# Kernel tuning notes

Measured on AMD Instinct MI355X. Metric: run time of the kernel, lower is better.

Reference implementation:

```python
import jax, jax.numpy as jnp
import numpy as np

B, C, H, W = 4, 1024, 14, 14
L = 80          # num labels / graph nodes
WD = 300        # word embedding dim
INTER = 1024    # semantic intermediary dim
OUT = 2048      # output_dim
TIME_STEP = 3


def setup_inputs() -> dict:
    key = jax.random.key(0)
    ks = jax.random.split(key, 24)
    s = 0.02  # weight scale to keep gates/tanh in sane range
    return {
        "img_feature_map": jax.random.normal(ks[0], (B, C, H, W), jnp.float32),
        "word_embedding": jax.random.normal(ks[1], (L, WD), jnp.float32),
        "adjacency": jax.random.uniform(ks[2], (L, L), jnp.float32) / L,
        "fc1_w": jax.random.normal(ks[3], (INTER, C), jnp.float32) * s,
        "fc2_w": jax.random.normal(ks[4], (INTER, WD), jnp.float32) * s,
        "fc3_w": jax.random.normal(ks[5], (INTER, INTER), jnp.float32) * s,
        "fc3_b": jnp.zeros((INTER,), jnp.float32),
        "fca_w": jax.random.normal(ks[6], (1, INTER), jnp.float32) * s,
        "fca_b": jnp.zeros((1,), jnp.float32),
        "w3": jax.random.normal(ks[7], (C, 2 * C), jnp.float32) * s,
        "b3": jnp.zeros((C,), jnp.float32),
        "u3": jax.random.normal(ks[8], (C, C), jnp.float32) * s,
        "u3b": jnp.zeros((C,), jnp.float32),
        "w4": jax.random.normal(ks[9], (C, 2 * C), jnp.float32) * s,
        "b4": jnp.zeros((C,), jnp.float32),
        "w5": jax.random.normal(ks[10], (C, 2 * C), jnp.float32) * s,
        "b5": jnp.zeros((C,), jnp.float32),
        "u5": jax.random.normal(ks[11], (C, C), jnp.float32) * s,
        "u5b": jnp.zeros((C,), jnp.float32),
        "fco_w": jax.random.normal(ks[12], (OUT, 2 * C), jnp.float32) * s,
        "fco_b": jnp.zeros((OUT,), jnp.float32),
    }


def _semantic(fmap, word_emb, fc1_w, fc2_w, fc3_w, fc3_b, fca_w, fca_b):
    # Faithful to torch: view(-1, C) on a contiguous (B,C,H,W) tensor is a raw
    # row-major reinterpret (NOT a BHWC transpose). jnp.reshape matches.
    b, c, h, w = fmap.shape
    x = fmap.reshape(-1, c)                                   # (B*H*W, C)
    f_wh = x @ fc1_w.T                                        # (N, INTER)
    f_wd = word_emb @ fc2_w.T                                 # (L, INTER)
    lb = jnp.tanh(f_wh[:, None, :] * f_wd[None, :, :])        # (N, L, INTER)
    lb = lb @ fc3_w.T + fc3_b                                 # (N, L, INTER)
    coeff = lb @ fca_w.T + fca_b                              # (N, L, 1)
    coeff = coeff.reshape(b, L, h * w)                        # torch .view semantics
    coeff = jax.nn.softmax(coeff, axis=2)
    coeff = coeff.reshape(b, h, w, L)
    fmap_bhwc = fmap.reshape(b, h, w, c)                      # raw reinterpret, as torch
    return jnp.einsum('bhwl,bhwc->blc', coeff, fmap_bhwc)     # (B, L, C)


def _ggnn(nodes, adj, w3, b3, u3, u3b, w4, b4, w5, b5, u5, u5b):
    for _ in range(TIME_STEP):
        a = jnp.einsum('nm,bmd->bnd', adj, nodes)             # in == out matrix
        av = jnp.concatenate([a, a], axis=-1)                 # (B, L, 2C)
        u3x = nodes @ u3.T + u3b
        z = jax.nn.sigmoid(av @ w3.T + b3 + u3x)
        r = jax.nn.sigmoid(av @ w4.T + b4 + u3x)              # torch bug: reuses fc_eq3_u
        hcand = jnp.tanh(av @ w5.T + b5 + (r * nodes) @ u5.T + u5b)
        nodes = (1.0 - z) * nodes + z * hcand
    return nodes


def reference(img_feature_map, word_embedding, adjacency,
              fc1_w, fc2_w, fc3_w, fc3_b, fca_w, fca_b,
              w3, b3, u3, u3b, w4, b4, w5, b5, u5, u5b,
              fco_w, fco_b):
    g = _semantic(img_feature_map, word_embedding,
                  fc1_w, fc2_w, fc3_w, fc3_b, fca_w, fca_b)   # (B, L, C)
    nodes = _ggnn(g, adjacency, w3, b3, u3, u3b, w4, b4, w5, b5, u5, u5b)
    feat = jnp.concatenate([nodes, g], axis=-1)               # (B, L, 2C)
    out = jnp.tanh(feat @ fco_w.T + fco_b)                    # (B, L, OUT)
    return out
```

## Files before the change

kernel.cpp:

```cpp
#include <hip/hip_runtime.h>
#include <hip/hip_bf16.h>

#define LL 80
#define NPIX 784
#define PBATCH 15680

#define DI __device__ __forceinline__

typedef short s8v __attribute__((ext_vector_type(8)));
typedef short short4v __attribute__((ext_vector_type(4)));
typedef float f32x4 __attribute__((ext_vector_type(4)));

DI float b2f(__hip_bfloat16 x) { return __bfloat162float(x); }
DI float s2f(short h) { return __uint_as_float(((unsigned int)(unsigned short)h) << 16); }

DI short f2b(float x) {
    unsigned int b = __float_as_uint(x);
    b += 0x7fffu + ((b >> 16) & 1u);
    return (short)(b >> 16);
}

template <int F> DI float LD(const void* p, int i) {
    if (F) return ((const float*)p)[i];
    return b2f(((const __hip_bfloat16*)p)[i]);
}

DI float fast_tanh(float x) {
    float e = __expf(2.0f * x);
    return 1.0f - 2.0f / (e + 1.0f);
}
DI float fast_sigmoid(float x) { return 1.0f / (1.0f + __expf(-x)); }

__global__ __launch_bounds__(256) void detect_dtype(const void* probe, int n, int* flag) {
    __shared__ int bad;
    if (threadIdx.x == 0) bad = 0;
    __syncthreads();
    int c = 0;
    for (int i = threadIdx.x; i < n; i += 256) {
        float v = b2f(((const __hip_bfloat16*)probe)[i]);
        if (!(fabsf(v) < 1000.0f)) c++;
    }
    if (c) atomicAdd(&bad, c);
    __syncthreads();
    if (threadIdx.x == 0) *flag = (bad > 8) ? 1 : 0;
}

DI void cvt_part(int f, const void* src, short* __restrict__ dst, int blk, int n) {
    int i0 = (blk * 256 + threadIdx.x) * 4;
    if (i0 >= n) return;
    if (f) {
        float4 v = *(const float4*)((const float*)src + i0);
        short4v o = { f2b(v.x), f2b(v.y), f2b(v.z), f2b(v.w) };
        *(short4v*)(dst + i0) = o;
    } else {
        *(short4v*)(dst + i0) = *(const short4v*)((const short*)src + i0);
    }
}

DI void wcat_part(int f, const void* w3, const void* w4, const void* w5, const void* u3,
                  short* __restrict__ wcat, int blk) {
    int i0 = (blk * 256 + threadIdx.x) * 4;
    int nr = i0 >> 10, k = i0 & 1023;
    int j = nr >> 10, r = nr & 1023;
    const void* W = (j == 0) ? w3 : (j == 1) ? w4 : (j == 2) ? w5 : u3;
    float4 v;
    if (j < 3) {
        if (f) {
            float4 x = *(const float4*)((const float*)W + r * 2048 + k);
            float4 y = *(const float4*)((const float*)W + r * 2048 + 1024 + k);
            v.x = x.x + y.x; v.y = x.y + y.y; v.z = x.z + y.z; v.w = x.w + y.w;
        } else {
            const short* Ws = (const short*)W;
            short4v x = *(const short4v*)(Ws + r * 2048 + k);
            short4v y = *(const short4v*)(Ws + r * 2048 + 1024 + k);
            v.x = s2f(x.x) + s2f(y.x); v.y = s2f(x.y) + s2f(y.y);
            v.z = s2f(x.z) + s2f(y.z); v.w = s2f(x.w) + s2f(y.w);
        }
    } else {
        if (f) v = *(const float4*)((const float*)W + r * 1024 + k);
        else {
            short4v x = *(const short4v*)((const short*)W + r * 1024 + k);
            v.x = s2f(x.x); v.y = s2f(x.y); v.z = s2f(x.z); v.w = s2f(x.w);
        }
    }
    short4v o = { f2b(v.x), f2b(v.y), f2b(v.z), f2b(v.w) };
    *(short4v*)(wcat + i0) = o;
}

template <int F>
DI void prep_u_part(const void* fc3_w, const void* fc3_b,
                    const void* fca_w, const void* fca_b,
                    float* u, float* c0, float* red, int blk) {
    if (blk < 4) {
        int k = blk * 256 + threadIdx.x;
        float acc = 0.f;
        for (int j = 0; j < 1024; j++)
            acc += LD<F>(fca_w, j) * LD<F>(fc3_w, j * 1024 + k);
        u[k] = acc;
    } else {
        float acc = 0.f;
        for (int j = threadIdx.x; j < 1024; j += 256)
            acc += LD<F>(fc3_b, j) * LD<F>(fca_w, j);
        red[threadIdx.x] = acc;
        __syncthreads();
        for (int s = 128; s > 0; s >>= 1) {
            if (threadIdx.x < s) red[threadIdx.x] += red[threadIdx.x + s];
            __syncthreads();
        }
        if (threadIdx.x == 0) *c0 = red[0] + LD<F>(fca_b, 0);
    }
}

template <int F>
DI void fc2_part(float* lds, const void* word, const void* fc2_w, float* C, int bx, int by) {
    float* As = lds;
    float* Ws2 = lds + 1088;
    const int tid = threadIdx.x;
    const int tx = tid & 15, ty = tid >> 4;
    const int m0 = by * 64, n0 = bx * 64;
    const int M = 80, K = 300;
    float acc[4][4] = {};

    for (int k0 = 0; k0 < K; k0 += 16) {
#pragma unroll
        for (int i = 0; i < 4; i++) {
            int idx = tid + i * 256;
            int kk = idx & 15, mm = idx >> 4;
            int m = m0 + mm, k = k0 + kk;
            As[kk * 68 + mm] = (m < M && k < K) ? LD<F>(word, m * 300 + k) : 0.f;
        }
#pragma unroll
        for (int i = 0; i < 4; i++) {
            int idx = tid + i * 256;
            int kk = idx & 15, nn = idx >> 4;
            int n = n0 + nn, k = k0 + kk;
            Ws2[kk * 68 + nn] = (k < K) ? LD<F>(fc2_w, n * 300 + k) : 0.f;
        }
        __syncthreads();
#pragma unroll
        for (int kk = 0; kk < 16; kk++) {
            float4 av = *(const float4*)(&As[kk * 68 + ty * 4]);
            float4 wv = *(const float4*)(&Ws2[kk * 68 + tx * 4]);
            float a4[4] = {av.x, av.y, av.z, av.w};
            float w4[4] = {wv.x, wv.y, wv.z, wv.w};
#pragma unroll
            for (int i = 0; i < 4; i++)
#pragma unroll
                for (int j = 0; j < 4; j++)
                    acc[i][j] += a4[i] * w4[j];
        }
        __syncthreads();
    }

    for (int i = 0; i < 4; i++) {
        int m = m0 + ty * 4 + i;
        if (m >= M) continue;
        for (int j = 0; j < 4; j++)
            C[m * 1024 + n0 + tx * 4 + j] = acc[i][j];
    }
}

__global__ __launch_bounds__(256) void mega_prep(
    const int* flag,
    const void* fmap, const void* fc1_w, const void* u5w,
    const void* w3, const void* w4, const void* w5, const void* u3,
    const void* fc3_w, const void* fc3_b, const void* fca_w, const void* fca_b,
    const void* word, const void* fc2_w,
    short* fmap_b, short* fc1w_b, short* u5w_b, short* wcat_b,
    float* u, float* c0, float* f_wd) {
    __shared__ float lds[2176];
    int f = *flag;
    int bid = blockIdx.x;
    if      (bid < 784)  cvt_part(f, fmap,  fmap_b, bid,        802816);
    else if (bid < 1808) cvt_part(f, fc1_w, fc1w_b, bid - 784,  1048576);
    else if (bid < 2832) cvt_part(f, u5w,   u5w_b,  bid - 1808, 1048576);
    else if (bid < 6928) wcat_part(f, w3, w4, w5, u3, wcat_b, bid - 2832);
    else if (bid < 6933) {
        if (f) prep_u_part<1>(fc3_w, fc3_b, fca_w, fca_b, u, c0, lds, bid - 6928);
        else   prep_u_part<0>(fc3_w, fc3_b, fca_w, fca_b, u, c0, lds, bid - 6928);
    } else {
        int r = bid - 6933;
        if (f) fc2_part<1>(lds, word, fc2_w, f_wd, r & 15, r >> 4);
        else   fc2_part<0>(lds, word, fc2_w, f_wd, r & 15, r >> 4);
    }
}

__global__ __launch_bounds__(256) void cvt_k(const int* flag, const void* src,
                                             short* __restrict__ dst, int n) {
    cvt_part(*flag, src, dst, blockIdx.x, n);
}

DI void mcore_b(const short* __restrict__ A, int lda,
                const short* __restrict__ B, int ldb,
                float* __restrict__ C, int ldc,
                int M, int kb, int ke, int m0, int n0) {
    __shared__ short As[4][64][8];
    __shared__ short Ws[4][64][8];
    const int tid = threadIdx.x;
    const int wv = tid >> 6, lane = tid & 63;
    const int mA = tid & 63, qA = tid >> 6;
    f32x4 acc[4] = {};

    for (int k0 = kb; k0 < ke; k0 += 32) {
        s8v va = {0,0,0,0,0,0,0,0};
        int gm = m0 + mA;
        if (gm < M) va = *(const s8v*)(A + gm * lda + k0 + 8 * qA);
        *(s8v*)&As[mA >> 4][(mA & 15) | (qA << 4)][0] = va;
        s8v vb = *(const s8v*)(B + (n0 + mA) * ldb + k0 + 8 * qA);
        *(s8v*)&Ws[mA >> 4][(mA & 15) | (qA << 4)][0] = vb;
        __syncthreads();
        s8v af = *(const s8v*)&As[wv][lane][0];
#pragma unroll
        for (int nf = 0; nf < 4; nf++) {
            s8v bf = *(const s8v*)&Ws[nf][lane][0];
            acc[nf] = __builtin_amdgcn_mfma_f32_16x16x32_bf16(af, bf, acc[nf], 0, 0, 0);
        }
        __syncthreads();
    }

    const int q = lane >> 4, cc = lane & 15;
#pragma unroll
    for (int nf = 0; nf < 4; nf++) {
        int n = n0 + 16 * nf + cc;
#pragma unroll
        for (int r = 0; r < 4; r++) {
            int m = m0 + 16 * wv + q * 4 + r;
            if (m < M) C[m * ldc + n] = acc[nf][r];
        }
    }
}

__global__ __launch_bounds__(256) void mfma_fc1(
    const short* __restrict__ fmap_b, const short* __restrict__ fc1w_b,
    float* __restrict__ fhP) {
    int z = blockIdx.z;
    mcore_b(fmap_b, 1024, fc1w_b, 1024, fhP + z * 802816, 1024,
            NPIX, z * 512, z * 512 + 512, blockIdx.y * 64, blockIdx.x * 64);
}

__global__ __launch_bounds__(256) void mfma_gate(
    const short* __restrict__ a_b, const short* __restrict__ nodes_b,
    const short* __restrict__ wcat_b, float* __restrict__ gP) {
    int z = blockIdx.z;
    const short* A = (blockIdx.x >= 48) ? nodes_b : a_b;
    mcore_b(A, 1024, wcat_b, 1024, gP + z * 1310720, 4096,
            320, z * 512, z * 512 + 512, blockIdx.y * 64, blockIdx.x * 64);
}

__global__ __launch_bounds__(256) void mfma_u5(
    const short* __restrict__ rn_b, const short* __restrict__ u5w_b,
    float* __restrict__ u5P) {
    int z = blockIdx.z;
    mcore_b(rn_b, 1024, u5w_b, 1024, u5P + z * 327680, 1024,
            320, z * 256, z * 256 + 256, blockIdx.y * 64, blockIdx.x * 64);
}

__global__ __launch_bounds__(256) void mfma_fin(
    const short* __restrict__ nodes_b, const short* __restrict__ g_b,
    const short* __restrict__ fcow_b, float* __restrict__ finP) {
    int z = blockIdx.z;
    const short* A = z ? (g_b - 1024) : nodes_b;
    mcore_b(A, 1024, fcow_b, 2048, finP + z * 655360, 2048,
            320, z * 1024, z * 1024 + 1024, blockIdx.y * 64, blockIdx.x * 64);
}

__global__ void fin_combine(const int* flag, const float* __restrict__ finP,
                            const void* fco_b, void* out, int n) {
    int i4 = (blockIdx.x * 256 + threadIdx.x) * 4;
    if (i4 >= n) return;
    int c = i4 & 2047;
    float4 p0 = *(const float4*)(finP + i4);
    float4 p1 = *(const float4*)(finP + 655360 + i4);
    int f = *flag;
    float v0 = fast_tanh(p0.x + p1.x + (f ? LD<1>(fco_b, c)   : LD<0>(fco_b, c)));
    float v1 = fast_tanh(p0.y + p1.y + (f ? LD<1>(fco_b, c+1) : LD<0>(fco_b, c+1)));
    float v2 = fast_tanh(p0.z + p1.z + (f ? LD<1>(fco_b, c+2) : LD<0>(fco_b, c+2)));
    float v3 = fast_tanh(p0.w + p1.w + (f ? LD<1>(fco_b, c+3) : LD<0>(fco_b, c+3)));
    if (f) {
        float4 o = {v0, v1, v2, v3};
        *(float4*)((float*)out + i4) = o;
    } else {
        short4v o = { f2b(v0), f2b(v1), f2b(v2), f2b(v3) };
        *(short4v*)((short*)out + i4) = o;
    }
}

__global__ __launch_bounds__(256) void coeff_kernel(
    const float* __restrict__ fhP, const float* __restrict__ f_wd,
    const float* __restrict__ u, const float* __restrict__ c0p,
    float* __restrict__ s) {
    int n = blockIdx.x;
    __shared__ float4 fh4[256];
    __shared__ float4 uu4[256];
    int t = threadIdx.x;
    {
        float4 a0 = *(const float4*)(fhP + n * 1024 + t * 4);
        float4 a1 = *(const float4*)(fhP + 802816 + n * 1024 + t * 4);
        float4 fv = {a0.x + a1.x, a0.y + a1.y, a0.z + a1.z, a0.w + a1.w};
        fh4[t] = fv;
        uu4[t] = *(const float4*)(u + t * 4);
    }
    __syncthreads();
    float c0 = *c0p;
    int wave = t >> 6, lane = t & 63;
    int b = n / 196, hw = n % 196;
    int l0 = blockIdx.y * 40;
    for (int l = l0 + wave; l < l0 + 40; l += 4) {
        const float4* fd4 = (const float4*)(f_wd + l * 1024);
        float p = 0.f;
#pragma unroll
        for (int k = 0; k < 4; k++) {
            int idx = lane + k * 64;
            float4 h = fh4[idx];
            float4 d = fd4[idx];
            float4 uu = uu4[idx];
            p += fast_tanh(h.x * d.x) * uu.x;
            p += fast_tanh(h.y * d.y) * uu.y;
            p += fast_tanh(h.z * d.z) * uu.z;
            p += fast_tanh(h.w * d.w) * uu.w;
        }
        for (int off = 32; off > 0; off >>= 1) p += __shfl_down(p, off);
        if (lane == 0) s[b * PBATCH + hw * LL + l] = p + c0;
    }
}

__global__ __launch_bounds__(64) void softmax196(float* __restrict__ s) {
    float* p = s + blockIdx.x * 196;
    int lane = threadIdx.x;
    float v[4];
    float mx = -1e30f;
#pragma unroll
    for (int i = 0; i < 4; i++) {
        int idx = lane + i * 64;
        v[i] = (idx < 196) ? p[idx] : -1e30f;
        mx = fmaxf(mx, v[i]);
    }
    for (int off = 32; off > 0; off >>= 1) mx = fmaxf(mx, __shfl_down(mx, off));
    mx = __shfl(mx, 0);
    float sum = 0.f;
#pragma unroll
    for (int i = 0; i < 4; i++) {
        int idx = lane + i * 64;
        if (idx < 196) { v[i] = __expf(v[i] - mx); sum += v[i]; }
    }
    for (int off = 32; off > 0; off >>= 1) sum += __shfl_down(sum, off);
    sum = __shfl(sum, 0);
    float inv = 1.f / sum;
#pragma unroll
    for (int i = 0; i < 4; i++) {
        int idx = lane + i * 64;
        if (idx < 196) p[idx] = v[i] * inv;
    }
}

__global__ __launch_bounds__(256) void g_kernel(
    const float* __restrict__ s, const short* __restrict__ fmap_b,
    float* __restrict__ nodes, short* __restrict__ nodes_b, short* __restrict__ g_b) {
    int bl = blockIdx.x;
    int b = bl / LL, l = bl % LL;
    __shared__ float co[196];
    for (int i = threadIdx.x; i < 196; i += 256)
        co[i] = s[b * PBATCH + i * LL + l];
    __syncthreads();
    int c4 = threadIdx.x * 4;
    const short* base = fmap_b + b * 196 * 1024 + c4;
    float a0 = 0.f, a1 = 0.f, a2 = 0.f, a3 = 0.f;
    for (int hw = 0; hw < 196; hw++) {
        short4v v = *(const short4v*)(base + hw * 1024);
        float w = co[hw];
        a0 += w * s2f(v.x); a1 += w * s2f(v.y);
        a2 += w * s2f(v.z); a3 += w * s2f(v.w);
    }
    int o = bl * 1024 + c4;
    float4 fa = {a0, a1, a2, a3};
    *(float4*)(nodes + o) = fa;
    short4v bb = { f2b(a0), f2b(a1), f2b(a2), f2b(a3) };
    *(short4v*)(nodes_b + o) = bb;
    *(short4v*)(g_b + o) = bb;
}

template <int F>
DI void adj_core(float* arw, const void* adj, const float* nodes, short* a_b) {
    int bl = blockIdx.x;
    int b = bl / LL, l = bl % LL;
    if (threadIdx.x < LL) arw[threadIdx.x] = LD<F>(adj, l * LL + threadIdx.x);
    __syncthreads();
    int c4 = threadIdx.x * 4;
    const float* nb = nodes + b * LL * 1024 + c4;
    float a0 = 0.f, a1 = 0.f, a2 = 0.f, a3 = 0.f;
    for (int m = 0; m < LL; m++) {
        float am = arw[m];
        float4 nd = *(const float4*)(nb + m * 1024);
        a0 += am * nd.x; a1 += am * nd.y; a2 += am * nd.z; a3 += am * nd.w;
    }
    short4v bb = { f2b(a0), f2b(a1), f2b(a2), f2b(a3) };
    *(short4v*)(a_b + bl * 1024 + c4) = bb;
}

__global__ __launch_bounds__(256) void adj_kernel(
    const int* flag, const void* adj, const float* nodes, short* a_b) {
    __shared__ float arw[LL];
    if (*flag) adj_core<1>(arw, adj, nodes, a_b);
    else       adj_core<0>(arw, adj, nodes, a_b);
}

template <int F>
DI void ew_r_core(const float* gP, const float* nodes,
                  const void* b4, const void* u3b, short* rn_b, int i4) {
    int m = i4 >> 10, c = i4 & 1023;
    int base = m * 4096;
    float4 r0 = *(const float4*)(gP + base + 1024 + c);
    float4 r1 = *(const float4*)(gP + 1310720 + base + 1024 + c);
    float4 x0 = *(const float4*)(gP + base + 3072 + c);
    float4 x1 = *(const float4*)(gP + 1310720 + base + 3072 + c);
    float4 nd = *(const float4*)(nodes + i4);
    short4v o;
    o.x = f2b(fast_sigmoid(r0.x + r1.x + x0.x + x1.x + LD<F>(b4, c)   + LD<F>(u3b, c))   * nd.x);
    o.y = f2b(fast_sigmoid(r0.y + r1.y + x0.y + x1.y + LD<F>(b4, c+1) + LD<F>(u3b, c+1)) * nd.y);
    o.z = f2b(fast_sigmoid(r0.z + r1.z + x0.z + x1.z + LD<F>(b4, c+2) + LD<F>(u3b, c+2)) * nd.z);
    o.w = f2b(fast_sigmoid(r0.w + r1.w + x0.w + x1.w + LD<F>(b4, c+3) + LD<F>(u3b, c+3)) * nd.w);
    *(short4v*)(rn_b + i4) = o;
}

__global__ void ew_r(const int* flag, const float* gP, const float* nodes,
                     const void* b4, const void* u3b, short* rn_b, int n) {
    int i4 = (blockIdx.x * 256 + threadIdx.x) * 4;
    if (i4 >= n) return;
    if (*flag) ew_r_core<1>(gP, nodes, b4, u3b, rn_b, i4);
    else       ew_r_core<0>(gP, nodes, b4, u3b, rn_b, i4);
}

template <int F>
DI void ewu(const float* gP, const float* u5P,
            const void* b3, const void* u3b, const void* b5, const void* u5b,
            float* nodes, short* nodes_b, int i4) {
    int m = i4 >> 10, c = i4 & 1023;
    int base = m * 4096;
    float4 z0 = *(const float4*)(gP + base + c);
    float4 z1 = *(const float4*)(gP + 1310720 + base + c);
    float4 h0 = *(const float4*)(gP + base + 2048 + c);
    float4 h1 = *(const float4*)(gP + 1310720 + base + 2048 + c);
    float4 x0 = *(const float4*)(gP + base + 3072 + c);
    float4 x1 = *(const float4*)(gP + 1310720 + base + 3072 + c);
    float4 u0 = *(const float4*)(u5P + i4);
    float4 u1 = *(const float4*)(u5P + 327680 + i4);
    float4 u2 = *(const float4*)(u5P + 655360 + i4);
    float4 u3v = *(const float4*)(u5P + 983040 + i4);
    float4 nd = *(const float4*)(nodes + i4);
    float4 out;
#define EWU1(CH, CO) { \
    float z = fast_sigmoid(z0.CH + z1.CH + x0.CH + x1.CH + LD<F>(b3, c+CO) + LD<F>(u3b, c+CO)); \
    float h = fast_tanh(h0.CH + h1.CH + u0.CH + u1.CH + u2.CH + u3v.CH + LD<F>(b5, c+CO) + LD<F>(u5b, c+CO)); \
    out.CH = (1.f - z) * nd.CH + z * h; }
    EWU1(x, 0) EWU1(y, 1) EWU1(z, 2) EWU1(w, 3)
#undef EWU1
    *(float4*)(nodes + i4) = out;
    short4v bb = { f2b(out.x), f2b(out.y), f2b(out.z), f2b(out.w) };
    *(short4v*)(nodes_b + i4) = bb;
}

__global__ void ew_upd(const int* flag, const float* gP, const float* u5P,
                       const void* b3, const void* u3b, const void* b5, const void* u5b,
                       float* nodes, short* nodes_b, int n) {
    int i4 = (blockIdx.x * 256 + threadIdx.x) * 4;
    if (i4 >= n) return;
    if (*flag) ewu<1>(gP, u5P, b3, u3b, b5, u5b, nodes, nodes_b, i4);
    else       ewu<0>(gP, u5P, b3, u3b, b5, u5b, nodes, nodes_b, i4);
}

extern "C" void kernel_launch(void* const* d_in, const int* in_sizes, int n_in,
                              void* d_out, int out_size, void* d_ws, size_t ws_size,
                              hipStream_t stream) {
    const void* fmap  = d_in[0];
    const void* word  = d_in[1];
    const void* adjm  = d_in[2];
    const void* fc1_w = d_in[3];
    const void* fc2_w = d_in[4];
    const void* fc3_w = d_in[5];
    const void* fc3_b = d_in[6];
    const void* fca_w = d_in[7];
    const void* fca_b = d_in[8];
    const void* w3    = d_in[9];
    const void* b3    = d_in[10];
    const void* u3    = d_in[11];
    const void* u3b   = d_in[12];
    const void* w4    = d_in[13];
    const void* b4    = d_in[14];
    const void* w5    = d_in[15];
    const void* b5    = d_in[16];
    const void* u5    = d_in[17];
    const void* u5b   = d_in[18];
    const void* fco_w = d_in[19];
    const void* fco_b = d_in[20];

    int*   flag    = (int*)d_ws;
    float* P       = (float*)d_ws + 16;
    float* nodes   = P;                       P += 327680;
    short* nodes_b = (short*)P;               P += 163840;
    short* g_b     = (short*)P;               P += 163840;
    short* a_b     = (short*)P;               P += 163840;
    short* rn_b    = (short*)P;               P += 163840;
    short* u5w_b   = (short*)P;               P += 524288;
    short* wcat_b  = (short*)P;               P += 2097152;
    float* R       = P;
    float* fhP    = R;
    float* f_wd   = R + 1605632;
    float* u      = f_wd + 81920;
    float* c0     = u + 1024;
    float* s      = c0 + 16;
    short* fmap_b = (short*)(s + 62720);
    short* fc1w_b = (short*)(s + 62720 + 401408);
    float* gP     = R;
    float* u5P    = R + 2621440;
    float* finP   = R;
    short* fcow_b = (short*)(R + 1310720);

    detect_dtype<<<1, 256, 0, stream>>>(fc1_w, 4096, flag);

    mega_prep<<<6965, 256, 0, stream>>>(flag, fmap, fc1_w, u5,
                                        w3, w4, w5, u3,
                                        fc3_w, fc3_b, fca_w, fca_b,
                                        word, fc2_w,
                                        fmap_b, fc1w_b, u5w_b, wcat_b,
                                        u, c0, f_wd);

    mfma_fc1<<<dim3(16, 13, 2), 256, 0, stream>>>(fmap_b, fc1w_b, fhP);
    coeff_kernel<<<dim3(NPIX, 2), 256, 0, stream>>>(fhP, f_wd, u, c0, s);
    softmax196<<<320, 64, 0, stream>>>(s);
    g_kernel<<<320, 256, 0, stream>>>(s, fmap_b, nodes, nodes_b, g_b);

    for (int t = 0; t < 3; t++) {
        adj_kernel<<<320, 256, 0, stream>>>(flag, adjm, nodes, a_b);
        mfma_gate<<<dim3(64, 5, 2), 256, 0, stream>>>(a_b, nodes_b, wcat_b, gP);
        ew_r<<<320, 256, 0, stream>>>(flag, gP, nodes, b4, u3b, rn_b, 327680);
        mfma_u5<<<dim3(16, 5, 4), 256, 0, stream>>>(rn_b, u5w_b, u5P);
        ew_upd<<<320, 256, 0, stream>>>(flag, gP, u5P, b3, u3b, b5, u5b,
                                        nodes, nodes_b, 327680);
    }

    cvt_k<<<4096, 256, 0, stream>>>(flag, fco_w, fcow_b, 4194304);
    mfma_fin<<<dim3(32, 5, 2), 256, 0, stream>>>(nodes_b, g_b, fcow_b, finP);
    fin_combine<<<640, 256, 0, stream>>>(flag, finP, fco_b, d_out, 655360);
}
```

Measured before the change: 399.3 us.

## Split fc3 projection across blocks and move fc2 GEMM to MFMA

Breaks the serial 1024-length reduction in the u-vector prep into 64 partial blocks, each summing 64 rows, and reduces the partials inside the fused semantic MFMA kernel. Replaces the scalar FP32 fc2 tile GEMM with a bf16 conversion padded to K=320, then runs it through the shared MFMA core alongside fc1. The aim is to remove the long-tail blocks in the prep kernel that serialize on a few workgroups. It adds extra padding conversions and partial buffers, and computes fc2 at bf16 precision.

```diff
diff --git a/kernel.cpp b/kernel.cpp
--- a/kernel.cpp
+++ b/kernel.cpp
@@ -55,6 +55,23 @@
     } else {
         *(short4v*)(dst + i0) = *(const short4v*)((const short*)src + i0);
     }
+}
+
+DI void cvt_pad(int f, const void* src, short* __restrict__ dst, int blk, int n) {
+    int i0 = (blk * 256 + threadIdx.x) * 4;
+    if (i0 >= n) return;
+    int row = i0 / 320;
+    int k = i0 - row * 320;
+    short4v o = {0, 0, 0, 0};
+    if (k < 300) {
+        if (f) {
+            float4 v = *(const float4*)((const float*)src + row * 300 + k);
+            o.x = f2b(v.x); o.y = f2b(v.y); o.z = f2b(v.z); o.w = f2b(v.w);
+        } else {
+            o = *(const short4v*)((const short*)src + row * 300 + k);
+        }
+    }
+    *(short4v*)(dst + i0) = o;
 }
 
 DI void wcat_part(int f, const void* w3, const void* w4, const void* w5, const void* u3,
@@ -88,76 +105,30 @@
 }
 
 template <int F>
-DI void prep_u_part(const void* fc3_w, const void* fc3_b,
-                    const void* fca_w, const void* fca_b,
-                    float* u, float* c0, float* red, int blk) {
-    if (blk < 4) {
-        int k = blk * 256 + threadIdx.x;
-        float acc = 0.f;
-        for (int j = 0; j < 1024; j++)
-            acc += LD<F>(fca_w, j) * LD<F>(fc3_w, j * 1024 + k);
-        u[k] = acc;
-    } else {
-        float acc = 0.f;
-        for (int j = threadIdx.x; j < 1024; j += 256)
-            acc += LD<F>(fc3_b, j) * LD<F>(fca_w, j);
-        red[threadIdx.x] = acc;
+DI void prep_upart(const void* fc3_w, const void* fca_w,
+                   float* __restrict__ u_part, int blk) {
+    int kseg = blk >> 4, jseg = blk & 15;
+    int k = kseg * 256 + threadIdx.x;
+    int j0 = jseg * 64;
+    float acc = 0.f;
+    for (int j = j0; j < j0 + 64; j++)
+        acc += LD<F>(fca_w, j) * LD<F>(fc3_w, j * 1024 + k);
+    u_part[jseg * 1024 + k] = acc;
+}
+
+template <int F>
+DI void prep_c0(const void* fc3_b, const void* fca_w, const void* fca_b,
+                float* c0, float* red) {
+    float acc = 0.f;
+    for (int j = threadIdx.x; j < 1024; j += 256)
+        acc += LD<F>(fc3_b, j) * LD<F>(fca_w, j);
+    red[threadIdx.x] = acc;
+    __syncthreads();
+    for (int s = 128; s > 0; s >>= 1) {
+        if (threadIdx.x < s) red[threadIdx.x] += red[threadIdx.x + s];
         __syncthreads();
-        for (int s = 128; s > 0; s >>= 1) {
-            if (threadIdx.x < s) red[threadIdx.x] += red[threadIdx.x + s];
-            __syncthreads();
-        }
-        if (threadIdx.x == 0) *c0 = red[0] + LD<F>(fca_b, 0);
-    }
-}
-
-template <int F>
-DI void fc2_part(float* lds, const void* word, const void* fc2_w, float* C, int bx, int by) {
-    float* As = lds;
-    float* Ws2 = lds + 1088;
-    const int tid = threadIdx.x;
-    const int tx = tid & 15, ty = tid >> 4;
-    const int m0 = by * 64, n0 = bx * 64;
-    const int M = 80, K = 300;
-    float acc[4][4] = {};
-
-    for (int k0 = 0; k0 < K; k0 += 16) {
-#pragma unroll
-        for (int i = 0; i < 4; i++) {
-            int idx = tid + i * 256;
-            int kk = idx & 15, mm = idx >> 4;
-            int m = m0 + mm, k = k0 + kk;
-            As[kk * 68 + mm] = (m < M && k < K) ? LD<F>(word, m * 300 + k) : 0.f;
-        }
-#pragma unroll
-        for (int i = 0; i < 4; i++) {
-            int idx = tid + i * 256;
-            int kk = idx & 15, nn = idx >> 4;
-            int n = n0 + nn, k = k0 + kk;
-            Ws2[kk * 68 + nn] = (k < K) ? LD<F>(fc2_w, n * 300 + k) : 0.f;
-        }
-        __syncthreads();
-#pragma unroll
-        for (int kk = 0; kk < 16; kk++) {
-            float4 av = *(const float4*)(&As[kk * 68 + ty * 4]);
-            float4 wv = *(const float4*)(&Ws2[kk * 68 + tx * 4]);
-            float a4[4] = {av.x, av.y, av.z, av.w};
-            float w4[4] = {wv.x, wv.y, wv.z, wv.w};
-#pragma unroll
-            for (int i = 0; i < 4; i++)
-#pragma unroll
-                for (int j = 0; j < 4; j++)
-                    acc[i][j] += a4[i] * w4[j];
-        }
-        __syncthreads();
-    }
-
-    for (int i = 0; i < 4; i++) {
-        int m = m0 + ty * 4 + i;
-        if (m >= M) continue;
-        for (int j = 0; j < 4; j++)
-            C[m * 1024 + n0 + tx * 4 + j] = acc[i][j];
-    }
+    }
+    if (threadIdx.x == 0) *c0 = red[0] + LD<F>(fca_b, 0);
 }
 
 __global__ __launch_bounds__(256) void mega_prep(
@@ -167,22 +138,24 @@
     const void* fc3_w, const void* fc3_b, const void* fca_w, const void* fca_b,
     const void* word, const void* fc2_w,
     short* fmap_b, short* fc1w_b, short* u5w_b, short* wcat_b,
-    float* u, float* c0, float* f_wd) {
-    __shared__ float lds[2176];
+    short* word_b, short* fc2w_b,
+    float* u_part, float* c0) {
+    __shared__ float red[256];
     int f = *flag;
     int bid = blockIdx.x;
     if      (bid < 784)  cvt_part(f, fmap,  fmap_b, bid,        802816);
     else if (bid < 1808) cvt_part(f, fc1_w, fc1w_b, bid - 784,  1048576);
     else if (bid < 2832) cvt_part(f, u5w,   u5w_b,  bid - 1808, 1048576);
     else if (bid < 6928) wcat_part(f, w3, w4, w5, u3, wcat_b, bid - 2832);
-    else if (bid < 6933) {
-        if (f) prep_u_part<1>(fc3_w, fc3_b, fca_w, fca_b, u, c0, lds, bid - 6928);
-        else   prep_u_part<0>(fc3_w, fc3_b, fca_w, fca_b, u, c0, lds, bid - 6928);
-    } else {
-        int r = bid - 6933;
-        if (f) fc2_part<1>(lds, word, fc2_w, f_wd, r & 15, r >> 4);
-        else   fc2_part<0>(lds, word, fc2_w, f_wd, r & 15, r >> 4);
-    }
+    else if (bid < 6992) {
+        if (f) prep_upart<1>(fc3_w, fca_w, u_part, bid - 6928);
+        else   prep_upart<0>(fc3_w, fca_w, u_part, bid - 6928);
+    } else if (bid == 6992) {
+        if (f) prep_c0<1>(fc3_b, fca_w, fca_b, c0, red);
+        else   prep_c0<0>(fc3_b, fca_w, fca_b, c0, red);
+    }
+    else if (bid < 7018) cvt_pad(f, word,  word_b, bid - 6993, 25600);
+    else                 cvt_pad(f, fc2_w, fc2w_b, bid - 7018, 327680);
 }
 
 __global__ __launch_bounds__(256) void cvt_k(const int* flag, const void* src,
@@ -230,12 +203,29 @@
     }
 }
 
-__global__ __launch_bounds__(256) void mfma_fc1(
+__global__ __launch_bounds__(256) void mfma_sem(
     const short* __restrict__ fmap_b, const short* __restrict__ fc1w_b,
-    float* __restrict__ fhP) {
-    int z = blockIdx.z;
-    mcore_b(fmap_b, 1024, fc1w_b, 1024, fhP + z * 802816, 1024,
-            NPIX, z * 512, z * 512 + 512, blockIdx.y * 64, blockIdx.x * 64);
+    const short* __restrict__ word_b, const short* __restrict__ fc2w_b,
+    const float* __restrict__ u_part, float* __restrict__ u,
+    float* __restrict__ fhP, float* __restrict__ f_wd) {
+    int bid = blockIdx.x;
+    if (bid < 416) {
+        int z = bid / 208, r = bid % 208;
+        int by = r / 16, bx = r % 16;
+        mcore_b(fmap_b, 1024, fc1w_b, 1024, fhP + z * 802816, 1024,
+                NPIX, z * 512, z * 512 + 512, by * 64, bx * 64);
+    } else if (bid < 448) {
+        int r = bid - 416;
+        int by = r >> 4, bx = r & 15;
+        mcore_b(word_b, 320, fc2w_b, 320, f_wd, 1024,
+                80, 0, 320, by * 64, bx * 64);
+    } else {
+        int k = (bid - 448) * 256 + threadIdx.x;
+        float a = 0.f;
+#pragma unroll
+        for (int s = 0; s < 16; s++) a += u_part[s * 1024 + k];
+        u[k] = a;
+    }
 }
 
 __global__ __launch_bounds__(256) void mfma_gate(
@@ -505,11 +495,14 @@
     float* R       = P;
     float* fhP    = R;
     float* f_wd   = R + 1605632;
-    float* u      = f_wd + 81920;
+    float* u_part = f_wd + 81920;
+    float* u      = u_part + 16384;
     float* c0     = u + 1024;
     float* s      = c0 + 16;
     short* fmap_b = (short*)(s + 62720);
-    short* fc1w_b = (short*)(s + 62720 + 401408);
+    short* fc1w_b = fmap_b + 802816;
+    short* word_b = fc1w_b + 1048576;
+    short* fc2w_b = word_b + 25600;
     float* gP     = R;
     float* u5P    = R + 2621440;
     float* finP   = R;
@@ -517,14 +510,15 @@
 
     detect_dtype<<<1, 256, 0, stream>>>(fc1_w, 4096, flag);
 
-    mega_prep<<<6965, 256, 0, stream>>>(flag, fmap, fc1_w, u5,
+    mega_prep<<<7338, 256, 0, stream>>>(flag, fmap, fc1_w, u5,
                                         w3, w4, w5, u3,
                                         fc3_w, fc3_b, fca_w, fca_b,
                                         word, fc2_w,
                                         fmap_b, fc1w_b, u5w_b, wcat_b,
-                                        u, c0, f_wd);
-
-    mfma_fc1<<<dim3(16, 13, 2), 256, 0, stream>>>(fmap_b, fc1w_b, fhP);
+                                        word_b, fc2w_b, u_part, c0);
+
+    mfma_sem<<<452, 256, 0, stream>>>(fmap_b, fc1w_b, word_b, fc2w_b,
+                                      u_part, u, fhP, f_wd);
     coeff_kernel<<<dim3(NPIX, 2), 256, 0, stream>>>(fhP, f_wd, u, c0, s);
     softmax196<<<320, 64, 0, stream>>>(s);
     g_kernel<<<320, 256, 0, stream>>>(s, fmap_b, nodes, nodes_b, g_b);
```

Result: faster. 359.5 us (-10.0%).
